# Kernel tuning notes

Hardware: AMD Instinct MI355X
Metric: run time of the kernel (lower is better)

Reference implementation:

```python
import jax, jax.numpy as jnp
import numpy as np

SPATIAL = ((100, 100), (50, 50), (25, 25), (13, 13))  # (h, w) per level
D_MODEL, H, L, P = 256, 8, 4, 4
HD = D_MODEL // H


def setup_inputs() -> dict:
    key = jax.random.key(0)
    ks = jax.random.split(key, 12)
    B = 2
    Lv = sum(h * w for h, w in SPATIAL)  # 13294
    Lq = Lv
    s = 0.02
    return {
        'query': jax.random.normal(ks[0], (B, Lq, D_MODEL), jnp.float32),
        'reference_points': jax.random.uniform(ks[1], (B, Lq, L, 2), jnp.float32),
        'value': jax.random.normal(ks[2], (B, Lv, D_MODEL), jnp.float32),
        'spatial_shapes': jnp.array(SPATIAL, jnp.int32),
        'W_off': jax.random.normal(ks[3], (D_MODEL, H * L * P * 2), jnp.float32) * s,
        'b_off': jax.random.normal(ks[4], (H * L * P * 2,), jnp.float32) * s,
        'W_attn': jax.random.normal(ks[5], (D_MODEL, H * L * P), jnp.float32) * s,
        'b_attn': jax.random.normal(ks[6], (H * L * P,), jnp.float32) * s,
        'W_v': jax.random.normal(ks[7], (D_MODEL, D_MODEL), jnp.float32) * s,
        'b_v': jax.random.normal(ks[8], (D_MODEL,), jnp.float32) * s,
        'W_out': jax.random.normal(ks[9], (D_MODEL, D_MODEL), jnp.float32) * s,
        'b_out': jax.random.normal(ks[10], (D_MODEL,), jnp.float32) * s,
    }


def _grid_sample_zeros(v, grid, h, w):
    # v: [N, HD, h*w] flattened feature map; grid: [N, Q, P, 2] in [-1, 1]
    # torch grid_sample bilinear, align_corners=False, padding_mode='zeros'
    x = (grid[..., 0] + 1.0) * (w * 0.5) - 0.5
    y = (grid[..., 1] + 1.0) * (h * 0.5) - 0.5
    x0 = jnp.floor(x); y0 = jnp.floor(y)
    x1 = x0 + 1.0;     y1 = y0 + 1.0
    wx1 = x - x0; wx0 = 1.0 - wx1
    wy1 = y - y0; wy0 = 1.0 - wy1

    def gather(xi, yi, wgt):
        valid = (xi >= 0) & (xi < w) & (yi >= 0) & (yi < h)
        xc = jnp.clip(xi, 0, w - 1).astype(jnp.int32)
        yc = jnp.clip(yi, 0, h - 1).astype(jnp.int32)
        idx = yc * w + xc                       # [N, Q, P]
        N, Q, Pp = idx.shape
        g = jnp.take_along_axis(v, idx.reshape(N, 1, Q * Pp), axis=2)
        g = g.reshape(N, v.shape[1], Q, Pp)     # [N, HD, Q, P]
        return g * (wgt * valid)[:, None, :, :]

    return (gather(x0, y0, wx0 * wy0) + gather(x1, y0, wx1 * wy0) +
            gather(x0, y1, wx0 * wy1) + gather(x1, y1, wx1 * wy1))


def reference(query, reference_points, value, spatial_shapes,
              W_off, b_off, W_attn, b_attn, W_v, b_v, W_out, b_out):
    B, Lq, _ = query.shape
    Lv = value.shape[1]
    v = (value @ W_v + b_v).reshape(B, Lv, H, HD)
    off = (query @ W_off + b_off).reshape(B, Lq, H, L, P, 2)
    aw = jax.nn.softmax((query @ W_attn + b_attn).reshape(B, Lq, H, L * P), axis=-1)
    # normalize offsets by (w, h) per level, add to reference points
    wh = jnp.array([[w_, h_] for h_, w_ in SPATIAL], jnp.float32)   # [L, 2]
    loc = reference_points[:, :, None, :, None, :] + off / wh[None, None, None, :, None, :]
    grids = 2.0 * loc - 1.0                                          # [B, Lq, H, L, P, 2]

    sampled = []
    start = 0
    for lid, (h_, w_) in enumerate(SPATIAL):
        n = h_ * w_
        vl = v[:, start:start + n].transpose(0, 2, 3, 1).reshape(B * H, HD, n)
        gl = grids[:, :, :, lid].transpose(0, 2, 1, 3, 4).reshape(B * H, Lq, P, 2)
        sampled.append(_grid_sample_zeros(vl, gl, h_, w_))           # [B*H, HD, Lq, P]
        start += n
    sv = jnp.concatenate(sampled, axis=-1)                           # [B*H, HD, Lq, L*P]
    awr = aw.transpose(0, 2, 1, 3).reshape(B * H, 1, Lq, L * P)
    out = (sv * awr).sum(-1)                                         # [B*H, HD, Lq]
    out = out.reshape(B, H, HD, Lq).transpose(0, 3, 1, 2).reshape(B, Lq, D_MODEL)
    return out @ W_out + b_out
```

## Files before the change

kernel.cpp:

```cpp
#include <hip/hip_runtime.h>
#include <hip/hip_bf16.h>
#include <math.h>


namespace {
constexpr int LQ    = 13294;
constexpr int LV    = 13294;
constexpr int NROWS = 2 * LQ;
}

typedef __attribute__((ext_vector_type(8))) short short8;
typedef __attribute__((ext_vector_type(4))) float f32x4;

__device__ inline float bf2f(unsigned u16) {
    union { unsigned u; float f; } c; c.u = u16 << 16; return c.f;
}
__device__ inline unsigned short f2bf(float f) {
    __hip_bfloat16 h = __float2bfloat16(f);
    return *reinterpret_cast<unsigned short*>(&h);
}

__global__ __launch_bounds__(256) void prep_weights(
    const float* __restrict__ Wv, const float* __restrict__ Woff,
    const float* __restrict__ Wattn, const float* __restrict__ Wout,
    __hip_bfloat16* __restrict__ WTf)
{
    const int c = blockIdx.x, k = threadIdx.x;
    float v;
    if (c < 256)      v = Wv[k * 256 + c];
    else if (c < 512) v = Woff[k * 256 + (c - 256)];
    else if (c < 640) v = Wattn[k * 128 + (c - 512)];
    else              v = Wout[k * 256 + (c - 640)];
    const int lane = (c & 15) | (((k >> 3) & 3) << 4);
    const size_t dst = ((size_t)((c >> 4) * 8 + (k >> 5)) * 64 + lane) * 8 + (k & 7);
    WTf[dst] = __float2bfloat16(v);
}

template<int NT, int OUTMODE, bool A_FP32>
__device__ __forceinline__ void gemm_core(
    short (*As)[264], const void* __restrict__ Xv,
    const __hip_bfloat16* __restrict__ WTf, int ct0,
    const float* __restrict__ bias, void* __restrict__ Yv,
    int ldY, int coloff, int M, int bx)
{
    const int t  = threadIdx.x;
    const int r0 = bx * 96;

    if (A_FP32) {
        const float* X = (const float*)Xv;
        #pragma unroll
        for (int i = 0; i < 24; ++i) {
            const int f4 = i * 256 + t;
            int row = r0 + (f4 >> 6);
            if (row >= M) row = M - 1;
            const int col4 = f4 & 63;
            const float4 u = *(const float4*)(X + (size_t)row * 256 + col4 * 4);
            union { unsigned short us[4]; uint2 v; } p;
            p.us[0] = f2bf(u.x); p.us[1] = f2bf(u.y);
            p.us[2] = f2bf(u.z); p.us[3] = f2bf(u.w);
            *(uint2*)(&As[f4 >> 6][col4 * 4]) = p.v;
        }
    } else {
        const __hip_bfloat16* X = (const __hip_bfloat16*)Xv;
        #pragma unroll
        for (int i = 0; i < 12; ++i) {
            const int f8 = i * 256 + t;
            int row = r0 + (f8 >> 5);
            if (row >= M) row = M - 1;
            const int c16 = f8 & 31;
            *(short8*)(&As[f8 >> 5][c16 * 8]) =
                *(const short8*)(X + (size_t)row * 256 + c16 * 8);
        }
    }
    __syncthreads();

    const int lane = t & 63;
    const int wv   = t >> 6;
    const int r16  = lane & 15;
    const int koff = (lane >> 4) * 8;

    f32x4 acc[6][NT];
    #pragma unroll
    for (int rt = 0; rt < 6; ++rt)
        #pragma unroll
        for (int nt = 0; nt < NT; ++nt)
            #pragma unroll
            for (int j = 0; j < 4; ++j) acc[rt][nt][j] = 0.f;

    #pragma unroll
    for (int kc = 0; kc < 8; ++kc) {
        short8 a[6];
        #pragma unroll
        for (int rt = 0; rt < 6; ++rt)
            a[rt] = *(const short8*)(&As[rt * 16 + r16][kc * 32 + koff]);
        #pragma unroll
        for (int nt = 0; nt < NT; ++nt) {
            const int ct = ct0 + wv * NT + nt;
            const short8 bfr =
                *(const short8*)(WTf + ((size_t)(ct * 8 + kc) * 64 + lane) * 8);
            #pragma unroll
            for (int rt = 0; rt < 6; ++rt)
                acc[rt][nt] = __builtin_amdgcn_mfma_f32_16x16x32_bf16(
                    a[rt], bfr, acc[rt][nt], 0, 0, 0);
        }
    }

    const int orow = (lane >> 4) * 4;
    #pragma unroll
    for (int rt = 0; rt < 6; ++rt)
    #pragma unroll
    for (int nt = 0; nt < NT; ++nt) {
        const int lcol = wv * (NT * 16) + nt * 16 + r16;
        const float bb = bias[lcol];
        #pragma unroll
        for (int j = 0; j < 4; ++j) {
            const int rr = r0 + rt * 16 + orow + j;
            if (rr < M) {
                const float v = acc[rt][nt][j] + bb;
                if (OUTMODE == 0) {
                    ((float*)Yv)[(size_t)rr * ldY + coloff + lcol] = v;
                } else if (OUTMODE == 1) {
                    ((__hip_bfloat16*)Yv)[(size_t)rr * ldY + coloff + lcol] =
                        __float2bfloat16(v);
                } else {
                    const int b  = (rr >= LQ) ? 1 : 0;
                    const int lv = rr - b * LQ;
                    const int h  = lcol >> 5, cc = lcol & 31;
                    ((__hip_bfloat16*)Yv)[(((size_t)(b * 8 + h)) * LV + lv) * 32 + cc] =
                        __float2bfloat16(v);
                }
            }
        }
    }
}

__global__ __launch_bounds__(256, 2) void gemm_vq(
    const float* __restrict__ value, const float* __restrict__ query,
    const __hip_bfloat16* __restrict__ WTf,
    const float* __restrict__ bv, const float* __restrict__ boff,
    const float* __restrict__ battn,
    __hip_bfloat16* __restrict__ vhm, __hip_bfloat16* __restrict__ offlog, int M)
{
    __shared__ short As[96][264];
    if (blockIdx.y == 0)
        gemm_core<4, 2, true>(As, value, WTf, 0,  bv,    vhm,    0,   0,   M, blockIdx.x);
    else if (blockIdx.y == 1)
        gemm_core<4, 1, true>(As, query, WTf, 16, boff,  offlog, 384, 0,   M, blockIdx.x);
    else
        gemm_core<2, 1, true>(As, query, WTf, 32, battn, offlog, 384, 256, M, blockIdx.x);
}

__global__ __launch_bounds__(256, 2) void gemm_out_k(
    const __hip_bfloat16* __restrict__ sampled, const __hip_bfloat16* __restrict__ WTf,
    const float* __restrict__ bout, float* __restrict__ out, int M)
{
    __shared__ short As[96][264];
    gemm_core<4, 0, false>(As, sampled, WTf, 40, bout, out, 256, 0, M, blockIdx.x);
}

__global__ __launch_bounds__(256) void ms_sample(
    const __hip_bfloat16* __restrict__ vhm, const __hip_bfloat16* __restrict__ offlog,
    const float* __restrict__ refpts, __hip_bfloat16* __restrict__ sampled)
{
    __shared__ char params[4][16][304];

    const int t    = threadIdx.x;
    const int row0 = blockIdx.x * 4;

    #pragma unroll
    for (int it = 0; it < 2; ++it) {
        const int sid = it * 256 + t;
        const int rl  = sid >> 7;
        const int h   = (sid >> 4) & 7;
        const int s   = sid & 15;
        const int row = row0 + rl;
        const int l   = s >> 2;
        const int wl  = (l == 0) ? 100 : (l == 1) ? 50 : (l == 2) ? 25 : 13;
        const int st  = (l == 0) ? 0 : (l == 1) ? 10000 : (l == 2) ? 12500 : 13125;
        const float wlf = (float)wl;

        const unsigned short* ol = (const unsigned short*)offlog + (size_t)row * 384;
        const unsigned uoff = *(const unsigned*)(ol + h * 32 + s * 2);
        const float ox = bf2f(uoff & 0xffffu), oy = bf2f(uoff >> 16);
        const float lg = bf2f(ol[256 + h * 16 + s]);
        const float2 rf = *(const float2*)(refpts + (size_t)row * 8 + l * 2);

        float m = lg;
        #pragma unroll
        for (int o = 8; o > 0; o >>= 1) m = fmaxf(m, __shfl_xor(m, o, 16));
        const float e = __expf(lg - m);
        float ssum = e;
        #pragma unroll
        for (int o = 8; o > 0; o >>= 1) ssum += __shfl_xor(ssum, o, 16);
        const float a = e / ssum;

        const float x = fmaf(rf.x, wlf, ox) - 0.5f;
        const float y = fmaf(rf.y, wlf, oy) - 0.5f;
        const float x0f = floorf(x), y0f = floorf(y);
        const int   x0 = (int)x0f, y0 = (int)y0f;
        const float wx1 = x - x0f, wx0 = 1.f - wx1;
        const float wy1 = y - y0f, wy0 = 1.f - wy1;
        const bool xv0 = (unsigned)x0       < (unsigned)wl;
        const bool xv1 = (unsigned)(x0 + 1) < (unsigned)wl;
        const bool yv0 = (unsigned)y0       < (unsigned)wl;
        const bool yv1 = (unsigned)(y0 + 1) < (unsigned)wl;
        const float ax0 = a * wx0, ax1 = a * wx1;
        float w00 = ax0 * wy0, w10 = ax1 * wy0;
        float w01 = ax0 * wy1, w11 = ax1 * wy1;
        w00 = (xv0 && yv0) ? w00 : 0.f;
        w10 = (xv1 && yv0) ? w10 : 0.f;
        w01 = (xv0 && yv1) ? w01 : 0.f;
        w11 = (xv1 && yv1) ? w11 : 0.f;
        const int cx0 = min(max(x0, 0), wl - 1);
        const int cx1 = min(max(x0 + 1, 0), wl - 1);
        const int cy0 = min(max(y0, 0), wl - 1);
        const int cy1 = min(max(y0 + 1, 0), wl - 1);
        const int r0b = (st + cy0 * wl) * 64;
        const int r1b = (st + cy1 * wl) * 64;
        uint4  offs; offs.x = r0b + cx0 * 64; offs.y = r0b + cx1 * 64;
                     offs.z = r1b + cx0 * 64; offs.w = r1b + cx1 * 64;
        float4 wv4;  wv4.x = w00; wv4.y = w10; wv4.z = w01; wv4.w = w11;
        char* pe = &params[rl][s][h * 32];
        *(uint4*)pe         = offs;
        *(float4*)(pe + 16) = wv4;
    }
    __syncthreads();

    const int rl  = t >> 6;
    const int h   = (t >> 3) & 7;
    const int c4  = t & 7;
    const int row = row0 + rl;
    const int b   = (row >= LQ) ? 1 : 0;
    const char* vbase = (const char*)vhm + ((size_t)((b << 3) + h) * LV) * 64 + c4 * 8;

    float a0 = 0.f, a1 = 0.f, a2 = 0.f, a3 = 0.f;

    #pragma unroll
    for (int sq = 0; sq < 4; ++sq) {
        uint4  of[4]; float4 w[4];
        #pragma unroll
        for (int i = 0; i < 4; ++i) {
            const char* pe = &params[rl][sq * 4 + i][h * 32];
            of[i] = *(const uint4*)pe;
            w[i]  = *(const float4*)(pe + 16);
        }
        uint2 q0[4], q1[4], q2[4], q3[4];
        #pragma unroll
        for (int i = 0; i < 4; ++i) {
            q0[i] = *(const uint2*)(vbase + of[i].x);
            q1[i] = *(const uint2*)(vbase + of[i].y);
            q2[i] = *(const uint2*)(vbase + of[i].z);
            q3[i] = *(const uint2*)(vbase + of[i].w);
        }
        #pragma unroll
        for (int i = 0; i < 4; ++i) {
            union { unsigned u; float f; } lo, hi;
            lo.u = q0[i].x << 16;          a0 = fmaf(lo.f, w[i].x, a0);
            hi.u = q0[i].x & 0xffff0000u;  a1 = fmaf(hi.f, w[i].x, a1);
            lo.u = q0[i].y << 16;          a2 = fmaf(lo.f, w[i].x, a2);
            hi.u = q0[i].y & 0xffff0000u;  a3 = fmaf(hi.f, w[i].x, a3);
            lo.u = q1[i].x << 16;          a0 = fmaf(lo.f, w[i].y, a0);
            hi.u = q1[i].x & 0xffff0000u;  a1 = fmaf(hi.f, w[i].y, a1);
            lo.u = q1[i].y << 16;          a2 = fmaf(lo.f, w[i].y, a2);
            hi.u = q1[i].y & 0xffff0000u;  a3 = fmaf(hi.f, w[i].y, a3);
            lo.u = q2[i].x << 16;          a0 = fmaf(lo.f, w[i].z, a0);
            hi.u = q2[i].x & 0xffff0000u;  a1 = fmaf(hi.f, w[i].z, a1);
            lo.u = q2[i].y << 16;          a2 = fmaf(lo.f, w[i].z, a2);
            hi.u = q2[i].y & 0xffff0000u;  a3 = fmaf(hi.f, w[i].z, a3);
            lo.u = q3[i].x << 16;          a0 = fmaf(lo.f, w[i].w, a0);
            hi.u = q3[i].x & 0xffff0000u;  a1 = fmaf(hi.f, w[i].w, a1);
            lo.u = q3[i].y << 16;          a2 = fmaf(lo.f, w[i].w, a2);
            hi.u = q3[i].y & 0xffff0000u;  a3 = fmaf(hi.f, w[i].w, a3);
        }
    }

    uint2 o;
    o.x = (unsigned)f2bf(a0) | ((unsigned)f2bf(a1) << 16);
    o.y = (unsigned)f2bf(a2) | ((unsigned)f2bf(a3) << 16);
    *(uint2*)((unsigned short*)sampled + (size_t)row * 256 + h * 32 + c4 * 4) = o;
}

extern "C" void kernel_launch(void* const* d_in, const int* in_sizes, int n_in,
                              void* d_out, int out_size, void* d_ws, size_t ws_size,
                              hipStream_t stream)
{
    const float* query  = (const float*)d_in[0];
    const float* refpts = (const float*)d_in[1];
    const float* value  = (const float*)d_in[2];
    const float* Woff   = (const float*)d_in[4];
    const float* boff   = (const float*)d_in[5];
    const float* Wattn  = (const float*)d_in[6];
    const float* battn  = (const float*)d_in[7];
    const float* Wv     = (const float*)d_in[8];
    const float* bv     = (const float*)d_in[9];
    const float* Wout   = (const float*)d_in[10];
    const float* bout   = (const float*)d_in[11];
    float* out = (float*)d_out;

    constexpr size_t SZ_VHM = (size_t)2 * 8 * LV * 32;
    constexpr size_t SZ_OFF = (size_t)NROWS * 384;
    constexpr size_t SZ_ROW = (size_t)NROWS * 256;
    __hip_bfloat16* ws      = (__hip_bfloat16*)d_ws;
    __hip_bfloat16* vhm     = ws;
    __hip_bfloat16* offlog  = vhm + SZ_VHM;
    __hip_bfloat16* sampled = offlog + SZ_OFF;
    __hip_bfloat16* WTf     = sampled + SZ_ROW;

    const int gblk = (NROWS + 95) / 96;
    const int sblk = NROWS / 4;

    hipLaunchKernelGGL(prep_weights, dim3(896), dim3(256), 0, stream,
                       Wv, Woff, Wattn, Wout, WTf);
    hipLaunchKernelGGL(gemm_vq, dim3(gblk, 3), dim3(256), 0, stream,
                       value, query, WTf, bv, boff, battn, vhm, offlog, NROWS);
    hipLaunchKernelGGL(ms_sample, dim3(sblk), dim3(256), 0, stream,
                       vhm, offlog, refpts, sampled);
    hipLaunchKernelGGL(gemm_out_k, dim3(gblk), dim3(256), 0, stream,
                       sampled, WTf, bout, out, NROWS);
}
```

Measured before the change: 131.9 us.

## Replace LDS-tiled GEMMs with per-wave direct-load MFMA and separate bf16 conversion

Adds a standalone kernel that converts value and query from fp32 to bf16 once. The GEMMs drop the shared-memory A tile: each wave owns one 16-row tile, holds its whole K-row of A in registers, and loops over all 16 (or 8) column tiles reading B straight from global memory. The goal is to remove LDS staging and barriers and the repeated fp32-to-bf16 conversion of query across two GEMM slices, and to raise occupancy. In exchange it adds an extra pass over memory for the conversion and cuts B-fragment reuse to one row tile per load, which raises global/L2 traffic for weights.

```diff
diff --git a/kernel.cpp b/kernel.cpp
--- a/kernel.cpp
+++ b/kernel.cpp
@@ -36,96 +36,77 @@
     WTf[dst] = __float2bfloat16(v);
 }
 
-template<int NT, int OUTMODE, bool A_FP32>
-__device__ __forceinline__ void gemm_core(
-    short (*As)[264], const void* __restrict__ Xv,
+__global__ __launch_bounds__(256) void conv_bf16(
+    const float* __restrict__ value, const float* __restrict__ query,
+    __hip_bfloat16* __restrict__ vbf, __hip_bfloat16* __restrict__ qbf)
+{
+    constexpr size_t NV = (size_t)NROWS * 256;
+    const size_t e = ((size_t)blockIdx.x * 256 + threadIdx.x) * 8;
+    if (e >= NV) return;
+    const float* src = (blockIdx.y == 0) ? value + e : query + e;
+    __hip_bfloat16* dst = (blockIdx.y == 0) ? vbf + e : qbf + e;
+    const float4 a = *(const float4*)src;
+    const float4 b = *(const float4*)(src + 4);
+    union { unsigned short us[8]; uint4 v; } o;
+    o.us[0] = f2bf(a.x); o.us[1] = f2bf(a.y); o.us[2] = f2bf(a.z); o.us[3] = f2bf(a.w);
+    o.us[4] = f2bf(b.x); o.us[5] = f2bf(b.y); o.us[6] = f2bf(b.z); o.us[7] = f2bf(b.w);
+    *(uint4*)dst = o.v;
+}
+
+template<int NTILES, int OUTMODE>
+__device__ __forceinline__ void gemm_direct_core(
+    const __hip_bfloat16* __restrict__ X,
     const __hip_bfloat16* __restrict__ WTf, int ct0,
     const float* __restrict__ bias, void* __restrict__ Yv,
-    int ldY, int coloff, int M, int bx)
-{
-    const int t  = threadIdx.x;
-    const int r0 = bx * 96;
-
-    if (A_FP32) {
-        const float* X = (const float*)Xv;
-        #pragma unroll
-        for (int i = 0; i < 24; ++i) {
-            const int f4 = i * 256 + t;
-            int row = r0 + (f4 >> 6);
-            if (row >= M) row = M - 1;
-            const int col4 = f4 & 63;
-            const float4 u = *(const float4*)(X + (size_t)row * 256 + col4 * 4);
-            union { unsigned short us[4]; uint2 v; } p;
-            p.us[0] = f2bf(u.x); p.us[1] = f2bf(u.y);
-            p.us[2] = f2bf(u.z); p.us[3] = f2bf(u.w);
-            *(uint2*)(&As[f4 >> 6][col4 * 4]) = p.v;
-        }
-    } else {
-        const __hip_bfloat16* X = (const __hip_bfloat16*)Xv;
-        #pragma unroll
-        for (int i = 0; i < 12; ++i) {
-            const int f8 = i * 256 + t;
-            int row = r0 + (f8 >> 5);
-            if (row >= M) row = M - 1;
-            const int c16 = f8 & 31;
-            *(short8*)(&As[f8 >> 5][c16 * 8]) =
-                *(const short8*)(X + (size_t)row * 256 + c16 * 8);
-        }
-    }
-    __syncthreads();
-
-    const int lane = t & 63;
-    const int wv   = t >> 6;
+    int ldY, int coloff, int M, int rt)
+{
+    const int lane = threadIdx.x & 63;
     const int r16  = lane & 15;
     const int koff = (lane >> 4) * 8;
-
-    f32x4 acc[6][NT];
-    #pragma unroll
-    for (int rt = 0; rt < 6; ++rt)
-        #pragma unroll
-        for (int nt = 0; nt < NT; ++nt)
-            #pragma unroll
-            for (int j = 0; j < 4; ++j) acc[rt][nt][j] = 0.f;
-
+    int rowA = rt * 16 + r16;
+    if (rowA >= M) rowA = M - 1;
+    const __hip_bfloat16* ap = X + (size_t)rowA * 256 + koff;
+
+    short8 a[8];
+    #pragma unroll
+    for (int kc = 0; kc < 8; ++kc)
+        a[kc] = *(const short8*)(ap + kc * 32);
+
+    f32x4 acc[NTILES];
+    #pragma unroll
+    for (int nt = 0; nt < NTILES; ++nt)
+        #pragma unroll
+        for (int j = 0; j < 4; ++j) acc[nt][j] = 0.f;
+
+    const __hip_bfloat16* bp = WTf + ((size_t)ct0 * 8 * 64 + lane) * 8;
     #pragma unroll
     for (int kc = 0; kc < 8; ++kc) {
-        short8 a[6];
-        #pragma unroll
-        for (int rt = 0; rt < 6; ++rt)
-            a[rt] = *(const short8*)(&As[rt * 16 + r16][kc * 32 + koff]);
-        #pragma unroll
-        for (int nt = 0; nt < NT; ++nt) {
-            const int ct = ct0 + wv * NT + nt;
-            const short8 bfr =
-                *(const short8*)(WTf + ((size_t)(ct * 8 + kc) * 64 + lane) * 8);
-            #pragma unroll
-            for (int rt = 0; rt < 6; ++rt)
-                acc[rt][nt] = __builtin_amdgcn_mfma_f32_16x16x32_bf16(
-                    a[rt], bfr, acc[rt][nt], 0, 0, 0);
+        #pragma unroll
+        for (int nt = 0; nt < NTILES; ++nt) {
+            const short8 bfr = *(const short8*)(bp + (size_t)(nt * 8 + kc) * 512);
+            acc[nt] = __builtin_amdgcn_mfma_f32_16x16x32_bf16(a[kc], bfr, acc[nt], 0, 0, 0);
         }
     }
 
     const int orow = (lane >> 4) * 4;
     #pragma unroll
-    for (int rt = 0; rt < 6; ++rt)
-    #pragma unroll
-    for (int nt = 0; nt < NT; ++nt) {
-        const int lcol = wv * (NT * 16) + nt * 16 + r16;
-        const float bb = bias[lcol];
+    for (int nt = 0; nt < NTILES; ++nt) {
+        const int col = nt * 16 + r16;
+        const float bb = bias[col];
         #pragma unroll
         for (int j = 0; j < 4; ++j) {
-            const int rr = r0 + rt * 16 + orow + j;
+            const int rr = rt * 16 + orow + j;
             if (rr < M) {
-                const float v = acc[rt][nt][j] + bb;
+                const float v = acc[nt][j] + bb;
                 if (OUTMODE == 0) {
-                    ((float*)Yv)[(size_t)rr * ldY + coloff + lcol] = v;
+                    ((float*)Yv)[(size_t)rr * ldY + coloff + col] = v;
                 } else if (OUTMODE == 1) {
-                    ((__hip_bfloat16*)Yv)[(size_t)rr * ldY + coloff + lcol] =
+                    ((__hip_bfloat16*)Yv)[(size_t)rr * ldY + coloff + col] =
                         __float2bfloat16(v);
                 } else {
                     const int b  = (rr >= LQ) ? 1 : 0;
                     const int lv = rr - b * LQ;
-                    const int h  = lcol >> 5, cc = lcol & 31;
+                    const int h  = col >> 5, cc = col & 31;
                     ((__hip_bfloat16*)Yv)[(((size_t)(b * 8 + h)) * LV + lv) * 32 + cc] =
                         __float2bfloat16(v);
                 }
@@ -134,28 +115,28 @@
     }
 }
 
-__global__ __launch_bounds__(256, 2) void gemm_vq(
-    const float* __restrict__ value, const float* __restrict__ query,
+__global__ __launch_bounds__(256, 3) void gemm_vq(
+    const __hip_bfloat16* __restrict__ vbf, const __hip_bfloat16* __restrict__ qbf,
     const __hip_bfloat16* __restrict__ WTf,
     const float* __restrict__ bv, const float* __restrict__ boff,
     const float* __restrict__ battn,
     __hip_bfloat16* __restrict__ vhm, __hip_bfloat16* __restrict__ offlog, int M)
 {
-    __shared__ short As[96][264];
+    const int rt = blockIdx.x * 4 + (threadIdx.x >> 6);
     if (blockIdx.y == 0)
-        gemm_core<4, 2, true>(As, value, WTf, 0,  bv,    vhm,    0,   0,   M, blockIdx.x);
+        gemm_direct_core<16, 2>(vbf, WTf, 0,  bv,    vhm,    0,   0,   M, rt);
     else if (blockIdx.y == 1)
-        gemm_core<4, 1, true>(As, query, WTf, 16, boff,  offlog, 384, 0,   M, blockIdx.x);
+        gemm_direct_core<16, 1>(qbf, WTf, 16, boff,  offlog, 384, 0,   M, rt);
     else
-        gemm_core<2, 1, true>(As, query, WTf, 32, battn, offlog, 384, 256, M, blockIdx.x);
-}
-
-__global__ __launch_bounds__(256, 2) void gemm_out_k(
+        gemm_direct_core<8,  1>(qbf, WTf, 32, battn, offlog, 384, 256, M, rt);
+}
+
+__global__ __launch_bounds__(256, 3) void gemm_out_k(
     const __hip_bfloat16* __restrict__ sampled, const __hip_bfloat16* __restrict__ WTf,
     const float* __restrict__ bout, float* __restrict__ out, int M)
 {
-    __shared__ short As[96][264];
-    gemm_core<4, 0, false>(As, sampled, WTf, 40, bout, out, 256, 0, M, blockIdx.x);
+    const int rt = blockIdx.x * 4 + (threadIdx.x >> 6);
+    gemm_direct_core<16, 0>(sampled, WTf, 40, bout, out, 256, 0, M, rt);
 }
 
 __global__ __launch_bounds__(256) void ms_sample(
@@ -303,16 +284,21 @@
     __hip_bfloat16* ws      = (__hip_bfloat16*)d_ws;
     __hip_bfloat16* vhm     = ws;
     __hip_bfloat16* offlog  = vhm + SZ_VHM;
-    __hip_bfloat16* sampled = offlog + SZ_OFF;
-    __hip_bfloat16* WTf     = sampled + SZ_ROW;
-
-    const int gblk = (NROWS + 95) / 96;
+    __hip_bfloat16* vbf     = offlog + SZ_OFF;
+    __hip_bfloat16* qbf     = vbf + SZ_ROW;
+    __hip_bfloat16* WTf     = qbf + SZ_ROW;
+    __hip_bfloat16* sampled = vbf;
+
+    const int cblk = (int)(((size_t)NROWS * 256 / 8 + 255) / 256);
+    const int gblk = (NROWS + 63) / 64;
     const int sblk = NROWS / 4;
 
     hipLaunchKernelGGL(prep_weights, dim3(896), dim3(256), 0, stream,
                        Wv, Woff, Wattn, Wout, WTf);
+    hipLaunchKernelGGL(conv_bf16, dim3(cblk, 2), dim3(256), 0, stream,
+                       value, query, vbf, qbf);
     hipLaunchKernelGGL(gemm_vq, dim3(gblk, 3), dim3(256), 0, stream,
-                       value, query, WTf, bv, boff, battn, vhm, offlog, NROWS);
+                       vbf, qbf, WTf, bv, boff, battn, vhm, offlog, NROWS);
     hipLaunchKernelGGL(ms_sample, dim3(sblk), dim3(256), 0, stream,
                        vhm, offlog, refpts, sampled);
     hipLaunchKernelGGL(gemm_out_k, dim3(gblk), dim3(256), 0, stream,
```

Result: slower. 154.6 us (+17.2%).
